# Kernel optimization log

Measured on AMD Instinct MI355X. Metric: run time of the kernel, lower is better.

Reference implementation:

```python
import jax, jax.numpy as jnp
import numpy as np

# YOLOLayer config (matches init_kwargs)
ANCHORS = [(0.1, 0.13), (0.3, 0.35), (0.6, 0.55)]  # (w, h) as fraction of image
NUM_CLASSES = 80
STRIDE = 8
NA = len(ANCHORS)


def setup_inputs() -> dict:
    key = jax.random.key(0)
    B, C, G = 16, NA * (NUM_CLASSES + 5), 64
    x = jax.random.normal(key, (B, C, G, G), dtype=jnp.float32)
    return {"x": x}


def reference(x):
    B = x.shape[0]
    g0, g1 = x.shape[2], x.shape[3]
    nC = NUM_CLASSES
    # [B, nA, g0, g1, 5+nC]
    pred = x.reshape(B, NA, nC + 5, g0, g1).transpose(0, 1, 3, 4, 2)
    sx = jax.nn.sigmoid(pred[..., 0])
    sy = jax.nn.sigmoid(pred[..., 1])
    w = pred[..., 2]
    h = pred[..., 3]
    pred_conf = jax.nn.sigmoid(pred[..., 4])
    pred_cls = jax.nn.sigmoid(pred[..., 5:])

    # grid offsets: grid_x varies along last dim, grid_y along dim -2 (torch semantics)
    grid_x = jnp.arange(g1, dtype=x.dtype)[None, None, None, :]
    grid_y = jnp.arange(g0, dtype=x.dtype)[None, None, :, None]
    scaled = jnp.asarray([(aw * g0, ah * g1) for aw, ah in ANCHORS], dtype=x.dtype)
    anchor_w = scaled[:, 0].reshape(1, NA, 1, 1)
    anchor_h = scaled[:, 1].reshape(1, NA, 1, 1)

    # torch uses .data (detached) for pred_boxes -> stop_gradient for faithfulness
    pred_boxes = jnp.stack(
        [sx + grid_x, sy + grid_y, jnp.exp(w) * anchor_w, jnp.exp(h) * anchor_h],
        axis=-1,
    )
    pred_boxes = jax.lax.stop_gradient(pred_boxes)

    boxes = pred_boxes.reshape(B, -1, 4) * STRIDE
    conf = pred_conf.reshape(B, -1, 1)
    cls = pred_cls.reshape(B, -1, nC)
    return boxes, conf, cls
```

## Files before the change

kernel.cpp:

```cpp
#include <hip/hip_runtime.h>
#include <stdint.h>


#define NB 16
#define NA 3
#define NC 80
#define GG 4096
#define CH 85
#define S  64
#define NG (CH * (S / 4))

__device__ __forceinline__ float sigmoidf(float v) {
    return 1.0f / (1.0f + __expf(-v));
}

__device__ __forceinline__ int lidx(int ch, int p) {
    int g = (p >> 2) ^ ((ch >> 2) & 7);
    return (ch << 6) + (g << 2) + (p & 3);
}

__global__ __launch_bounds__(256) void yolo_kernel(const float* __restrict__ x,
                                                   float* __restrict__ out) {
    __shared__ float lds[CH * S];

    const int blk  = blockIdx.x;
    const int tile = blk & 63;
    const int ba   = blk >> 6;
    const int a    = ba % NA;
    const int s0   = tile * S;
    const int tid  = threadIdx.x;
    const int lane = tid & 63;
    const int wv   = tid >> 6;

    const float* __restrict__ xin = x + (size_t)ba * CH * GG + s0;

    #pragma unroll
    for (int it = 0; it < 6; ++it) {
        int g0 = it * 256 + wv * 64;
        int g  = g0 + lane;
        if (g < NG) {
            int ch  = g >> 4;
            int p4  = g & 15;
            int sp4 = p4 ^ ((ch >> 2) & 7);
            const float* gp = xin + (size_t)ch * GG + (sp4 << 2);
            float* lp = &lds[g0 << 2];
            __builtin_amdgcn_global_load_lds(
                (const __attribute__((address_space(1))) void*)gp,
                (__attribute__((address_space(3))) void*)lp,
                16, 0, 0);
        }
    }
    __syncthreads();

    const float anchor_w[NA] = {0.1f * 64 * 8, 0.3f * 64 * 8, 0.6f * 64 * 8};
    const float anchor_h[NA] = {0.13f * 64 * 8, 0.35f * 64 * 8, 0.55f * 64 * 8};

    const int loc = ba * GG + s0;
    float* __restrict__ boxes = out;
    float* __restrict__ conf  = out + (size_t)NB * NA * GG * 4;
    float* __restrict__ cls   = out + (size_t)NB * NA * GG * 5;

    if (tid < S) {
        int p  = tid;
        int sp = s0 + p;
        float gx = (float)(sp & 63);
        float gy = (float)(sp >> 6);
        float4 bx;
        bx.x = (sigmoidf(lds[lidx(0, p)]) + gx) * 8.0f;
        bx.y = (sigmoidf(lds[lidx(1, p)]) + gy) * 8.0f;
        bx.z = __expf(lds[lidx(2, p)]) * anchor_w[a];
        bx.w = __expf(lds[lidx(3, p)]) * anchor_h[a];
        reinterpret_cast<float4*>(boxes)[loc + p] = bx;
        conf[loc + p] = sigmoidf(lds[lidx(4, p)]);
    }

    float4* __restrict__ cls4 =
        reinterpret_cast<float4*>(cls) + (size_t)loc * 20;
    #pragma unroll
    for (int i = tid; i < (S * 20); i += 256) {
        int p  = i / 20;
        int c4 = i % 20;
        int r  = 5 + (c4 << 2);
        float4 v;
        v.x = sigmoidf(lds[lidx(r + 0, p)]);
        v.y = sigmoidf(lds[lidx(r + 1, p)]);
        v.z = sigmoidf(lds[lidx(r + 2, p)]);
        v.w = sigmoidf(lds[lidx(r + 3, p)]);
        cls4[i] = v;
    }
}

extern "C" void kernel_launch(void* const* d_in, const int* in_sizes, int n_in,
                              void* d_out, int out_size, void* d_ws, size_t ws_size,
                              hipStream_t stream) {
    const float* x = (const float*)d_in[0];
    float* out = (float*)d_out;
    dim3 grid(NB * NA * (GG / S));
    yolo_kernel<<<grid, 256, 0, stream>>>(x, out);
}
```

Baseline: 25.83 us.

## Process four tiles per block with double-buffered async LDS staging

Each block now handles four consecutive spatial tiles instead of one and shrinks the grid to match. The global-to-LDS loads for the next tile are issued into a second LDS buffer while the current tile is computed and stored, with manual vmcnt waits and barriers controlling the handoff. The aim is to hide load latency in a bandwidth-bound kernel and amortize block launch cost. The cost is doubled LDS per block and a quarter as many blocks, which can lower occupancy and latency hiding. Correctness also depends on the hand-tuned vmcnt counts.

Result: faster. 25.17 us (-2.6%).

```diff
diff --git a/kernel.cpp b/kernel.cpp
--- a/kernel.cpp
+++ b/kernel.cpp
@@ -1,5 +1,4 @@
 #include <hip/hip_runtime.h>
-#include <stdint.h>
 
 
 #define NB 16
@@ -9,6 +8,9 @@
 #define CH 85
 #define S  64
 #define NG (CH * (S / 4))
+#define GPW (NG / 4)
+#define NT 4
+#define GRID (NB * NA * (GG / S) / NT)
 
 __device__ __forceinline__ float sigmoidf(float v) {
     return 1.0f / (1.0f + __expf(-v));
@@ -21,72 +23,93 @@
 
 __global__ __launch_bounds__(256) void yolo_kernel(const float* __restrict__ x,
                                                    float* __restrict__ out) {
-    __shared__ float lds[CH * S];
+    __shared__ float lds[2][CH * S];
 
-    const int blk  = blockIdx.x;
-    const int tile = blk & 63;
-    const int ba   = blk >> 6;
-    const int a    = ba % NA;
-    const int s0   = tile * S;
     const int tid  = threadIdx.x;
     const int lane = tid & 63;
     const int wv   = tid >> 6;
 
-    const float* __restrict__ xin = x + (size_t)ba * CH * GG + s0;
-
-    #pragma unroll
-    for (int it = 0; it < 6; ++it) {
-        int g0 = it * 256 + wv * 64;
-        int g  = g0 + lane;
-        if (g < NG) {
-            int ch  = g >> 4;
-            int p4  = g & 15;
-            int sp4 = p4 ^ ((ch >> 2) & 7);
-            const float* gp = xin + (size_t)ch * GG + (sp4 << 2);
-            float* lp = &lds[g0 << 2];
-            __builtin_amdgcn_global_load_lds(
-                (const __attribute__((address_space(1))) void*)gp,
-                (__attribute__((address_space(3))) void*)lp,
-                16, 0, 0);
-        }
-    }
-    __syncthreads();
-
-    const float anchor_w[NA] = {0.1f * 64 * 8, 0.3f * 64 * 8, 0.6f * 64 * 8};
-    const float anchor_h[NA] = {0.13f * 64 * 8, 0.35f * 64 * 8, 0.55f * 64 * 8};
-
-    const int loc = ba * GG + s0;
     float* __restrict__ boxes = out;
     float* __restrict__ conf  = out + (size_t)NB * NA * GG * 4;
     float* __restrict__ cls   = out + (size_t)NB * NA * GG * 5;
 
-    if (tid < S) {
-        int p  = tid;
-        int sp = s0 + p;
-        float gx = (float)(sp & 63);
-        float gy = (float)(sp >> 6);
-        float4 bx;
-        bx.x = (sigmoidf(lds[lidx(0, p)]) + gx) * 8.0f;
-        bx.y = (sigmoidf(lds[lidx(1, p)]) + gy) * 8.0f;
-        bx.z = __expf(lds[lidx(2, p)]) * anchor_w[a];
-        bx.w = __expf(lds[lidx(3, p)]) * anchor_h[a];
-        reinterpret_cast<float4*>(boxes)[loc + p] = bx;
-        conf[loc + p] = sigmoidf(lds[lidx(4, p)]);
-    }
+    auto stage = [&](int tg, int buf) {
+        const float* __restrict__ xin =
+            x + (size_t)(tg >> 6) * CH * GG + (tg & 63) * S;
+        #pragma unroll
+        for (int it = 0; it < 6; ++it) {
+            int g0 = wv * GPW + it * 64;
+            if (it * 64 + lane < GPW) {
+                int g   = g0 + lane;
+                int ch  = g >> 4;
+                int p4  = g & 15;
+                int sp4 = p4 ^ ((ch >> 2) & 7);
+                const float* gp = xin + (size_t)ch * GG + (sp4 << 2);
+                float* lp = &lds[buf][g0 << 2];
+                __builtin_amdgcn_global_load_lds(
+                    (const __attribute__((address_space(1))) void*)gp,
+                    (__attribute__((address_space(3))) void*)lp,
+                    16, 0, 0);
+            }
+        }
+    };
 
-    float4* __restrict__ cls4 =
-        reinterpret_cast<float4*>(cls) + (size_t)loc * 20;
+    auto compute = [&](int tg, int buf) {
+        const float* __restrict__ L = lds[buf];
+        const int ba  = tg >> 6;
+        const int a   = ba % NA;
+        const int s0  = (tg & 63) * S;
+        const int loc = ba * GG + s0;
+
+        const float anchor_w[NA] = {0.1f * 64 * 8, 0.3f * 64 * 8, 0.6f * 64 * 8};
+        const float anchor_h[NA] = {0.13f * 64 * 8, 0.35f * 64 * 8, 0.55f * 64 * 8};
+
+        if (tid < S) {
+            int p  = tid;
+            int sp = s0 + p;
+            float gx = (float)(sp & 63);
+            float gy = (float)(sp >> 6);
+            float4 bx;
+            bx.x = (sigmoidf(L[lidx(0, p)]) + gx) * 8.0f;
+            bx.y = (sigmoidf(L[lidx(1, p)]) + gy) * 8.0f;
+            bx.z = __expf(L[lidx(2, p)]) * anchor_w[a];
+            bx.w = __expf(L[lidx(3, p)]) * anchor_h[a];
+            reinterpret_cast<float4*>(boxes)[loc + p] = bx;
+            conf[loc + p] = sigmoidf(L[lidx(4, p)]);
+        }
+
+        float4* __restrict__ cls4 =
+            reinterpret_cast<float4*>(cls) + (size_t)loc * 20;
+        #pragma unroll
+        for (int i0 = 0; i0 < 5; ++i0) {
+            int i  = i0 * 256 + tid;
+            int p  = i / 20;
+            int c4 = i % 20;
+            int r  = 5 + (c4 << 2);
+            float4 v;
+            v.x = sigmoidf(L[lidx(r + 0, p)]);
+            v.y = sigmoidf(L[lidx(r + 1, p)]);
+            v.z = sigmoidf(L[lidx(r + 2, p)]);
+            v.w = sigmoidf(L[lidx(r + 3, p)]);
+            cls4[i] = v;
+        }
+    };
+
+    const int tg0 = blockIdx.x * NT;
+
+    stage(tg0, 0);
     #pragma unroll
-    for (int i = tid; i < (S * 20); i += 256) {
-        int p  = i / 20;
-        int c4 = i % 20;
-        int r  = 5 + (c4 << 2);
-        float4 v;
-        v.x = sigmoidf(lds[lidx(r + 0, p)]);
-        v.y = sigmoidf(lds[lidx(r + 1, p)]);
-        v.z = sigmoidf(lds[lidx(r + 2, p)]);
-        v.w = sigmoidf(lds[lidx(r + 3, p)]);
-        cls4[i] = v;
+    for (int k = 0; k < NT; ++k) {
+        if (k + 1 < NT) {
+            stage(tg0 + k + 1, (k + 1) & 1);
+            asm volatile("s_waitcnt vmcnt(6)" ::: "memory");
+        } else {
+            asm volatile("s_waitcnt vmcnt(0)" ::: "memory");
+        }
+        __builtin_amdgcn_s_barrier();
+        __builtin_amdgcn_sched_barrier(0);
+        compute(tg0 + k, k & 1);
+        __builtin_amdgcn_s_barrier();
     }
 }
 
@@ -95,6 +118,5 @@
                               hipStream_t stream) {
     const float* x = (const float*)d_in[0];
     float* out = (float*)d_out;
-    dim3 grid(NB * NA * (GG / S));
-    yolo_kernel<<<grid, 256, 0, stream>>>(x, out);
+    yolo_kernel<<<dim3(GRID), 256, 0, stream>>>(x, out);
 }
```

## Give each wave its own 64-pixel strip with double-buffered async LDS staging

Applied to the files above, without the earlier changes.

Work is split per wave: each wave owns 64 spatial positions, processed as four 16-position chunks. Chunks are loaded into per-wave double-buffered LDS with global_load_lds and ordered by explicit vmcnt waits instead of block-wide __syncthreads, so loading the next chunk overlaps computing the current one. The box output is written by all 64 lanes, one scalar component per lane. The change relies on hand-counted vmcnt values and a new XOR swizzle, and each load now moves smaller 16-position pieces, which risks less efficient memory transactions.

Result: slower. 31.41 us (+21.6%).

```diff
diff --git a/kernel.cpp b/kernel.cpp
--- a/kernel.cpp
+++ b/kernel.cpp
@@ -1,5 +1,4 @@
 #include <hip/hip_runtime.h>
-#include <stdint.h>
 
 
 #define NB 16
@@ -7,87 +6,107 @@
 #define NC 80
 #define GG 4096
 #define CH 85
-#define S  64
-#define NG (CH * (S / 4))
+#define SP 16
+#define NGW 340
+#define FLT 1360
 
 __device__ __forceinline__ float sigmoidf(float v) {
     return 1.0f / (1.0f + __expf(-v));
 }
 
-__device__ __forceinline__ int lidx(int ch, int p) {
-    int g = (p >> 2) ^ ((ch >> 2) & 7);
-    return (ch << 6) + (g << 2) + (p & 3);
-}
-
 __global__ __launch_bounds__(256) void yolo_kernel(const float* __restrict__ x,
                                                    float* __restrict__ out) {
-    __shared__ float lds[CH * S];
+    __shared__ float lds[4][2][FLT];
 
-    const int blk  = blockIdx.x;
-    const int tile = blk & 63;
-    const int ba   = blk >> 6;
-    const int a    = ba % NA;
-    const int s0   = tile * S;
     const int tid  = threadIdx.x;
     const int lane = tid & 63;
     const int wv   = tid >> 6;
+    const int W    = blockIdx.x * 4 + wv;
+    const int ba   = W >> 6;
+    const int a    = ba % NA;
+    const int base = (W & 63) << 6;
 
-    const float* __restrict__ xin = x + (size_t)ba * CH * GG + s0;
+    const float* __restrict__ xrow = x + (size_t)ba * CH * GG;
 
-    #pragma unroll
-    for (int it = 0; it < 6; ++it) {
-        int g0 = it * 256 + wv * 64;
-        int g  = g0 + lane;
-        if (g < NG) {
-            int ch  = g >> 4;
-            int p4  = g & 15;
-            int sp4 = p4 ^ ((ch >> 2) & 7);
-            const float* gp = xin + (size_t)ch * GG + (sp4 << 2);
-            float* lp = &lds[g0 << 2];
-            __builtin_amdgcn_global_load_lds(
-                (const __attribute__((address_space(1))) void*)gp,
-                (__attribute__((address_space(3))) void*)lp,
-                16, 0, 0);
+    float* __restrict__ boxesF = out;
+    float* __restrict__ conf   = out + (size_t)NB * NA * GG * 4;
+    float4* __restrict__ cls4  =
+        reinterpret_cast<float4*>(out + (size_t)NB * NA * GG * 5);
+
+    const float aw = (a == 0) ? 0.1f * 64 * 8 : (a == 1) ? 0.3f * 64 * 8 : 0.6f * 64 * 8;
+    const float ah = (a == 0) ? 0.13f * 64 * 8 : (a == 1) ? 0.35f * 64 * 8 : 0.55f * 64 * 8;
+
+    auto stage = [&](int k, int buf) {
+        const float* src = xrow + (base + k * SP);
+        #pragma unroll
+        for (int it = 0; it < 6; ++it) {
+            int g = it * 64 + lane;
+            if (g < NGW) {
+                int ch = g >> 2;
+                int q  = g & 3;
+                int sq = q ^ ((ch >> 2) & 3);
+                const float* gp = src + (size_t)ch * GG + (sq << 2);
+                float* lp = &lds[wv][buf][it * 256];
+                __builtin_amdgcn_global_load_lds(
+                    (const __attribute__((address_space(1))) void*)gp,
+                    (__attribute__((address_space(3))) void*)lp,
+                    16, 0, 0);
+            }
         }
-    }
-    __syncthreads();
+    };
 
-    const float anchor_w[NA] = {0.1f * 64 * 8, 0.3f * 64 * 8, 0.6f * 64 * 8};
-    const float anchor_h[NA] = {0.13f * 64 * 8, 0.35f * 64 * 8, 0.55f * 64 * 8};
+    auto compute = [&](int k, int buf) {
+        const float* __restrict__ L = lds[wv][buf];
+        const int s0  = base + k * SP;
+        const int loc = ba * GG + s0;
 
-    const int loc = ba * GG + s0;
-    float* __restrict__ boxes = out;
-    float* __restrict__ conf  = out + (size_t)NB * NA * GG * 4;
-    float* __restrict__ cls   = out + (size_t)NB * NA * GG * 5;
+        {
+            int p = lane >> 2, comp = lane & 3;
+            float v  = L[comp * 16 + p];
+            float e  = __expf(comp >= 2 ? v : -v);
+            float sg = 1.0f / (1.0f + e);
+            float gxy  = (comp == 0) ? (float)((s0 & 63) + p) : (float)(s0 >> 6);
+            float anch = (comp == 2) ? aw : ah;
+            float r = (comp < 2) ? (sg + gxy) * 8.0f : e * anch;
+            boxesF[(size_t)loc * 4 + lane] = r;
+            if (lane < SP)
+                conf[loc + lane] = sigmoidf(L[64 + (lane ^ 4)]);
+        }
 
-    if (tid < S) {
-        int p  = tid;
-        int sp = s0 + p;
-        float gx = (float)(sp & 63);
-        float gy = (float)(sp >> 6);
-        float4 bx;
-        bx.x = (sigmoidf(lds[lidx(0, p)]) + gx) * 8.0f;
-        bx.y = (sigmoidf(lds[lidx(1, p)]) + gy) * 8.0f;
-        bx.z = __expf(lds[lidx(2, p)]) * anchor_w[a];
-        bx.w = __expf(lds[lidx(3, p)]) * anchor_h[a];
-        reinterpret_cast<float4*>(boxes)[loc + p] = bx;
-        conf[loc + p] = sigmoidf(lds[lidx(4, p)]);
-    }
+        #pragma unroll
+        for (int it = 0; it < 5; ++it) {
+            int i  = it * 64 + lane;
+            int p  = i / 20;
+            int c4 = i - p * 20;
+            int r0 = 5 + (c4 << 2);
+            float4 v;
+            v.x = sigmoidf(L[(r0 + 0) * 16 + (p ^ ((r0 + 0) & 12))]);
+            v.y = sigmoidf(L[(r0 + 1) * 16 + (p ^ ((r0 + 1) & 12))]);
+            v.z = sigmoidf(L[(r0 + 2) * 16 + (p ^ ((r0 + 2) & 12))]);
+            v.w = sigmoidf(L[(r0 + 3) * 16 + (p ^ ((r0 + 3) & 12))]);
+            cls4[(size_t)loc * 20 + i] = v;
+        }
+    };
 
-    float4* __restrict__ cls4 =
-        reinterpret_cast<float4*>(cls) + (size_t)loc * 20;
-    #pragma unroll
-    for (int i = tid; i < (S * 20); i += 256) {
-        int p  = i / 20;
-        int c4 = i % 20;
-        int r  = 5 + (c4 << 2);
-        float4 v;
-        v.x = sigmoidf(lds[lidx(r + 0, p)]);
-        v.y = sigmoidf(lds[lidx(r + 1, p)]);
-        v.z = sigmoidf(lds[lidx(r + 2, p)]);
-        v.w = sigmoidf(lds[lidx(r + 3, p)]);
-        cls4[i] = v;
-    }
+    stage(0, 0);
+    stage(1, 1);
+    asm volatile("s_waitcnt vmcnt(6)" ::: "memory");
+    __builtin_amdgcn_sched_barrier(0);
+    compute(0, 0);
+
+    stage(2, 0);
+    asm volatile("s_waitcnt vmcnt(13)" ::: "memory");
+    __builtin_amdgcn_sched_barrier(0);
+    compute(1, 1);
+
+    stage(3, 1);
+    asm volatile("s_waitcnt vmcnt(13)" ::: "memory");
+    __builtin_amdgcn_sched_barrier(0);
+    compute(2, 0);
+
+    asm volatile("s_waitcnt vmcnt(0)" ::: "memory");
+    __builtin_amdgcn_sched_barrier(0);
+    compute(3, 1);
 }
 
 extern "C" void kernel_launch(void* const* d_in, const int* in_sizes, int n_in,
@@ -95,6 +114,5 @@
                               hipStream_t stream) {
     const float* x = (const float*)d_in[0];
     float* out = (float*)d_out;
-    dim3 grid(NB * NA * (GG / S));
-    yolo_kernel<<<grid, 256, 0, stream>>>(x, out);
+    yolo_kernel<<<dim3(768), 256, 0, stream>>>(x, out);
 }
```
